# Optimization experiments

Hardware: AMD Instinct MI355X
Metric: run time of the kernel (lower is better)

Reference implementation:

```python
import jax, jax.numpy as jnp
import numpy as np

N, E, B = 20000, 320000, 64
HID, DEPTH, NFREQ = 128, 4, 8
NODE_DIM, EDGE_DIM, SG = 4, 3, 230
TWO_PI = 2.0 * np.pi


def setup_inputs() -> dict:
    key = jax.random.key(0)
    ks = jax.random.split(key, 20)
    inp = {}
    inp["x"] = jax.random.normal(ks[0], (N, NODE_DIM), jnp.float32)
    inp["edge_index"] = jax.random.randint(ks[1], (2, E), 0, N)
    inp["edge_attr"] = jax.random.normal(ks[2], (E, EDGE_DIM), jnp.float32)
    inp["batch"] = jnp.sort(jax.random.randint(ks[3], (N,), 0, B))
    inp["space_group"] = jax.random.randint(ks[4], (B,), 0, SG)
    inp["node_w"] = jax.random.normal(ks[5], (NODE_DIM, HID), jnp.float32) * 0.1
    inp["node_b"] = jnp.zeros((HID,), jnp.float32)
    inp["sg_table"] = jax.random.normal(ks[6], (SG, HID), jnp.float32) * 0.1
    inp["lin_w"] = jax.random.normal(ks[7], (DEPTH, 2 * HID + EDGE_DIM, HID), jnp.float32) * 0.05
    inp["lin_b"] = jnp.zeros((DEPTH, HID), jnp.float32)
    inp["att_w"] = jax.random.normal(ks[8], (DEPTH, 2 * HID + EDGE_DIM), jnp.float32) * 0.05
    inp["att_b"] = jnp.zeros((DEPTH,), jnp.float32)
    inp["fk_w"] = jax.random.normal(ks[9], (DEPTH, NFREQ, HID, HID), jnp.float32) * 0.1
    inp["fk_b"] = jnp.zeros((DEPTH, HID), jnp.float32)
    inp["bn_g"] = jnp.ones((DEPTH, HID), jnp.float32)
    inp["bn_b"] = jnp.zeros((DEPTH, HID), jnp.float32)
    inp["pool_w"] = jax.random.normal(ks[10], (HID,), jnp.float32) * 0.1
    inp["pool_b"] = jnp.zeros((), jnp.float32)
    inp["head_w1"] = jax.random.normal(ks[11], (4, 2 * HID, HID), jnp.float32) * 0.05
    inp["head_b1"] = jnp.zeros((4, HID), jnp.float32)
    for i, (nm, od) in enumerate([("e", 1), ("s", 3), ("c", 7), ("m", 3)]):
        inp[nm + "_w2"] = jax.random.normal(ks[12 + i], (HID, od), jnp.float32) * 0.05
        inp[nm + "_b2"] = jnp.zeros((od,), jnp.float32)
    return inp


def reference(x, edge_index, edge_attr, batch, space_group, node_w, node_b, sg_table,
              lin_w, lin_b, att_w, att_b, fk_w, fk_b, bn_g, bn_b, pool_w, pool_b,
              head_w1, head_b1, e_w2, e_b2, s_w2, s_b2, c_w2, c_b2, m_w2, m_b2):
    src, dst = edge_index[0], edge_index[1]  # x_j = x[src], x_i = x[dst]
    h = x @ node_w + node_b                  # [N, HID]
    sg = sg_table[space_group]               # [B, HID]
    freqs = jnp.arange(1, NFREQ + 1, dtype=h.dtype)
    for l in range(DEPTH):
        # edge conv: gather-concat-linear-sigmoid attention-scatter add
        tmp = jnp.concatenate([h[dst], h[src], edge_attr], axis=-1)   # [E, 2H+3]
        alpha = jax.nn.sigmoid(tmp @ att_w[l] + att_b[l])[:, None]    # [E, 1]
        msg = alpha * (tmp @ lin_w[l] + lin_b[l])                     # [E, H]
        h_conv = jax.ops.segment_sum(msg, dst, num_segments=N)
        # Fourier-Kolmogorov branch
        ang = TWO_PI * freqs[None, :, None] * h[:, None, :]           # [N, K, H]
        h_fk = (jnp.einsum('nki,kio->no', jnp.sin(ang), fk_w[l])
                + jnp.einsum('nki,kio->no', jnp.cos(ang), fk_w[l]) + fk_b[l])
        h = h_conv + h_fk
        # BatchNorm1d (batch statistics, training semantics) + ReLU; dropout = identity (eval)
        mu = h.mean(axis=0)
        var = h.var(axis=0)
        h = (h - mu) / jnp.sqrt(var + 1e-5) * bn_g[l] + bn_b[l]
        h = jax.nn.relu(h)
    # attention pool: softmax over ALL nodes (dim=0), as in the original
    a = jax.nn.softmax(h @ pool_w + pool_b, axis=0)[:, None]          # [N, 1]
    pooled = jax.ops.segment_sum(a * h, batch, num_segments=B)        # [B, H]
    comb = jnp.concatenate([pooled, sg], axis=-1)                     # [B, 2H]

    def head(i, w2, b2):
        z = jax.nn.relu(comb @ head_w1[i] + head_b1[i])
        return z @ w2 + b2

    energy = head(0, e_w2, e_b2)          # [B, 1]
    stability = head(1, s_w2, s_b2)       # [B, 3]
    crystal_system = head(2, c_w2, c_b2)  # [B, 7]
    material_type = head(3, m_w2, m_b2)   # [B, 3]
    return energy, stability, crystal_system, material_type
```

## Files before the change

### kernel.cpp

```cpp
#include <hip/hip_runtime.h>
#include <math.h>

#define HID 128
#define DEPTH 4
#define PSPLIT 16
#define SMAXB 40

typedef _Float16 half8 __attribute__((ext_vector_type(8)));
typedef float f4 __attribute__((ext_vector_type(4)));

__global__ void k_node_embed(const float* __restrict__ x, const float* __restrict__ nw,
                             const float* __restrict__ nb, float* __restrict__ h, int N) {
    int idx = blockIdx.x * blockDim.x + threadIdx.x;
    if (idx >= N * HID) return;
    int n = idx >> 7, c = idx & 127;
    float acc = nb[c];
#pragma unroll
    for (int d = 0; d < 4; ++d) acc += x[n * 4 + d] * nw[d * HID + c];
    h[idx] = acc;
}

__global__ void k_wsplit(const float* __restrict__ fkw, _Float16* __restrict__ whi,
                         _Float16* __restrict__ wlo) {
    __shared__ float sh[64][65];
    int bid = blockIdx.x;
    int l = bid >> 5; int r = bid & 31; int kb = r >> 1; int nbk = r & 1;
    const float* W = fkw + (size_t)l * 131072;
    _Float16* Hl = whi + (size_t)l * 131072;
    _Float16* Ll = wlo + (size_t)l * 131072;
    int k0 = kb * 64, n0 = nbk * 64;
    for (int i = threadIdx.x; i < 4096; i += 256) {
        int kk = i >> 6, nn = i & 63;
        sh[kk][nn] = W[(k0 + kk) * HID + n0 + nn];
    }
    __syncthreads();
    for (int i = threadIdx.x; i < 4096; i += 256) {
        int nn = i >> 6, kk = i & 63;
        float w = sh[kk][nn];
        _Float16 hi = (_Float16)w;
        _Float16 lo = (_Float16)((w - (float)hi) * 2048.f);
        Hl[(n0 + nn) * 1024 + k0 + kk] = hi;
        Ll[(n0 + nn) * 1024 + k0 + kk] = lo;
    }
}

__global__ void k_hist(const int* __restrict__ dst, int* __restrict__ deg, int E) {
    int e = blockIdx.x * 256 + threadIdx.x;
    if (e < E) atomicAdd(&deg[dst[e]], 1);
}

__global__ void k_scan_a(const int* __restrict__ deg, int* __restrict__ bsum, int N) {
    __shared__ int sh[256];
    int i = blockIdx.x * 256 + threadIdx.x;
    sh[threadIdx.x] = (i < N) ? deg[i] : 0;
    __syncthreads();
    for (int off = 128; off > 0; off >>= 1) {
        if (threadIdx.x < (unsigned)off) sh[threadIdx.x] += sh[threadIdx.x + off];
        __syncthreads();
    }
    if (threadIdx.x == 0) bsum[blockIdx.x] = sh[0];
}

__global__ void k_scan_b(int* __restrict__ bsum, int nb) {
    __shared__ int sh[256];
    int v = (threadIdx.x < (unsigned)nb) ? bsum[threadIdx.x] : 0;
    sh[threadIdx.x] = v;
    __syncthreads();
    for (int off = 1; off < 256; off <<= 1) {
        int add = (threadIdx.x >= (unsigned)off) ? sh[threadIdx.x - off] : 0;
        __syncthreads();
        sh[threadIdx.x] += add;
        __syncthreads();
    }
    if (threadIdx.x < (unsigned)nb) bsum[threadIdx.x] = sh[threadIdx.x] - v;
}

__global__ void k_scan_c(const int* __restrict__ deg, const int* __restrict__ bsum,
                         int* __restrict__ offs, int* __restrict__ cursor, int N) {
    __shared__ int sh[256];
    int i = blockIdx.x * 256 + threadIdx.x;
    int v = (i < N) ? deg[i] : 0;
    sh[threadIdx.x] = v;
    __syncthreads();
    for (int off = 1; off < 256; off <<= 1) {
        int add = (threadIdx.x >= (unsigned)off) ? sh[threadIdx.x - off] : 0;
        __syncthreads();
        sh[threadIdx.x] += add;
        __syncthreads();
    }
    int ex = bsum[blockIdx.x] + sh[threadIdx.x] - v;
    if (i < N) { offs[i] = ex; cursor[i] = ex; }
    if (i == N - 1) offs[N] = ex + v;
}

__global__ void k_scatter(const int* __restrict__ src, const int* __restrict__ dst,
                          const float* __restrict__ ea, int* cursor,
                          int* __restrict__ srco, float4* __restrict__ ea3o, int E) {
    int e = blockIdx.x * 256 + threadIdx.x;
    if (e < E) {
        int d = dst[e];
        int p = atomicAdd(&cursor[d], 1);
        srco[p] = src[e];
        float4 q;
        q.x = ea[e * 3 + 0]; q.y = ea[e * 3 + 1]; q.z = ea[e * 3 + 2]; q.w = 0.f;
        ea3o[p] = q;
    }
}

__global__ void k_bstart(const int* __restrict__ batch, int* __restrict__ boffs, int N, int B) {
    int n = blockIdx.x * 256 + threadIdx.x;
    if (n >= N) return;
    int b1 = batch[n];
    if (n == 0) for (int b = 0; b <= b1; ++b) boffs[b] = 0;
    int b2 = (n + 1 < N) ? batch[n + 1] : B;
    for (int b = b1 + 1; b <= b2; ++b) boffs[b] = n + 1;
}

__global__ __launch_bounds__(256) void k_node_lin(const float* __restrict__ h,
                           const float* __restrict__ linw, const float* __restrict__ linb,
                           const float* __restrict__ attw, const float* __restrict__ attb,
                           float* __restrict__ A1, float* __restrict__ A2,
                           float* __restrict__ a1, float* __restrict__ a2, int N) {
    __shared__ float hT[HID][20];
    int nb = blockIdx.x * 16;
    int tid = threadIdx.x;
    for (int i = tid; i < 16 * HID; i += 256) {
        int n = i >> 7, c = i & 127;
        int gn = nb + n;
        hT[c][n] = (gn < N) ? h[gn * HID + c] : 0.f;
    }
    __syncthreads();
    {
        int node = tid >> 4, lane16 = tid & 15;
        float p1 = 0.f, p2 = 0.f;
#pragma unroll
        for (int j = 0; j < 8; ++j) {
            int k = lane16 * 8 + j;
            float hv = hT[k][node];
            p1 += hv * attw[k];
            p2 += hv * attw[128 + k];
        }
        for (int off = 8; off > 0; off >>= 1) {
            p1 += __shfl_down(p1, off, 16);
            p2 += __shfl_down(p2, off, 16);
        }
        int gn = nb + node;
        if (lane16 == 0 && gn < N) {
            a1[gn] = p1 + attb[0];
            a2[gn] = p2;
        }
    }
    int c = tid & 127, r = tid >> 7;
    const float* Wd = linw;
    const float* Ws = linw + 128 * HID;
    float acc1[8] = {0, 0, 0, 0, 0, 0, 0, 0}, acc2[8] = {0, 0, 0, 0, 0, 0, 0, 0};
#pragma unroll 4
    for (int k = 0; k < HID; ++k) {
        float wd = Wd[k * HID + c];
        float ws = Ws[k * HID + c];
        float4 h0 = *(const float4*)&hT[k][r * 8];
        float4 h1 = *(const float4*)&hT[k][r * 8 + 4];
        acc1[0] += h0.x * wd; acc2[0] += h0.x * ws;
        acc1[1] += h0.y * wd; acc2[1] += h0.y * ws;
        acc1[2] += h0.z * wd; acc2[2] += h0.z * ws;
        acc1[3] += h0.w * wd; acc2[3] += h0.w * ws;
        acc1[4] += h1.x * wd; acc2[4] += h1.x * ws;
        acc1[5] += h1.y * wd; acc2[5] += h1.y * ws;
        acc1[6] += h1.z * wd; acc2[6] += h1.z * ws;
        acc1[7] += h1.w * wd; acc2[7] += h1.w * ws;
    }
    float lb = linb[c];
#pragma unroll
    for (int j = 0; j < 8; ++j) {
        int gn = nb + r * 8 + j;
        if (gn < N) {
            A1[(size_t)gn * HID + c] = acc1[j] + lb;
            A2[(size_t)gn * HID + c] = acc2[j];
        }
    }
}

__global__ __launch_bounds__(256) void k_edge(const float* __restrict__ A1,
        const float* __restrict__ A2, const float* __restrict__ a1,
        const float* __restrict__ a2, const int* __restrict__ srco,
        const float4* __restrict__ ea3o, const int* __restrict__ offs,
        const float* __restrict__ linw3, const float* __restrict__ attw3,
        float* __restrict__ hconv, double* __restrict__ stats, int N) {
    __shared__ float part[8][HID + 4];
    int n = blockIdx.x;
    int tid = threadIdx.x;
    if (n == 0) stats[tid] = 0.0;
    int lane32 = tid & 31, slot = tid >> 5;
    int c4 = lane32 * 4;
    float4 w0v = *(const float4*)&linw3[c4];
    float4 w1v = *(const float4*)&linw3[HID + c4];
    float4 w2v = *(const float4*)&linw3[2 * HID + c4];
    float aw0 = attw3[0], aw1 = attw3[1], aw2 = attw3[2];
    float a1n = a1[n];
    float4 A1v = *(const float4*)&A1[(size_t)n * HID + c4];
    float4 acc; acc.x = acc.y = acc.z = acc.w = 0.f;
    int s0 = offs[n], s1 = offs[n + 1];
    for (int idx = s0 + slot; idx < s1; idx += 8) {
        int s = srco[idx];
        float4 q = ea3o[idx];
        float logit = a1n + a2[s] + q.x * aw0 + q.y * aw1 + q.z * aw2;
        float al = 1.f / (1.f + __expf(-logit));
        float4 a2v = *(const float4*)&A2[(size_t)s * HID + c4];
        float4 pre;
        pre.x = A1v.x + a2v.x + q.x * w0v.x + q.y * w1v.x + q.z * w2v.x;
        pre.y = A1v.y + a2v.y + q.x * w0v.y + q.y * w1v.y + q.z * w2v.y;
        pre.z = A1v.z + a2v.z + q.x * w0v.z + q.y * w1v.z + q.z * w2v.z;
        pre.w = A1v.w + a2v.w + q.x * w0v.w + q.y * w1v.w + q.z * w2v.w;
        acc.x += al * pre.x; acc.y += al * pre.y;
        acc.z += al * pre.z; acc.w += al * pre.w;
    }
    *(float4*)&part[slot][c4] = acc;
    __syncthreads();
    if (slot == 0) {
        float4 p = *(const float4*)&part[0][c4];
#pragma unroll
        for (int s = 1; s < 8; ++s) {
            float4 r = *(const float4*)&part[s][c4];
            p.x += r.x; p.y += r.y; p.z += r.z; p.w += r.w;
        }
        *(float4*)&hconv[(size_t)n * HID + c4] = p;
    }
}

#define FK_AST  264
__global__ __launch_bounds__(256) void k_fk(const float* __restrict__ h,
        const _Float16* __restrict__ whi, const _Float16* __restrict__ wlo,
        float* __restrict__ p0, float* __restrict__ p1,
        float* __restrict__ p2, float* __restrict__ p3, int N) {
    __shared__ _Float16 ahi[32 * FK_AST];
    __shared__ _Float16 alo[32 * FK_AST];
    int tid = threadIdx.x;
    int bx = blockIdx.x;
    int nb = (bx >> 2) * 32;
    int ks = bx & 3;
    int kbase = ks * 256;
    int fr0 = kbase >> 7;
    {
        int row = tid >> 3;
        int o8 = tid & 7;
        int gn = nb + row;
        int rc = (gn < N) ? gn : (N - 1);
        const float* hp = h + (size_t)rc * HID + o8 * 8;
        float hv[2][8];
        *(float4*)&hv[0][0] = *(const float4*)hp;
        *(float4*)&hv[0][4] = *(const float4*)(hp + 4);
        *(float4*)&hv[1][0] = *(const float4*)(hp + 64);
        *(float4*)&hv[1][4] = *(const float4*)(hp + 68);
#pragma unroll
        for (int g = 0; g < 2; ++g) {
            float freqf = 6.2831853f * (float)(fr0 + g + 1);
#pragma unroll
            for (int s = 0; s < 2; ++s) {
                half8 vh, vl;
#pragma unroll
                for (int j = 0; j < 8; ++j) {
                    float ang = freqf * hv[s][j] + 0.78539816f;
                    float a = 1.41421356f * __sinf(ang);
                    _Float16 hi = (_Float16)a;
                    vh[j] = hi;
                    vl[j] = (_Float16)((a - (float)hi) * 2048.f);
                }
                int oct = g * 16 + s * 8 + o8;
                *(half8*)&ahi[row * FK_AST + oct * 8] = vh;
                *(half8*)&alo[row * FK_AST + oct * 8] = vl;
            }
        }
    }
    __syncthreads();
    int lane = tid & 63, wv = tid >> 6;
    int quad = lane >> 4, l16 = lane & 15;
    int n0w = wv * 32;
    f4 acc0[2][2], accL[2][2];
#pragma unroll
    for (int mi = 0; mi < 2; ++mi)
#pragma unroll
        for (int ni = 0; ni < 2; ++ni) { acc0[mi][ni] = (f4)(0.f); accL[mi][ni] = (f4)(0.f); }
    const _Float16* bhp0 = whi + (size_t)(n0w + l16) * 1024 + kbase + quad * 8;
    const _Float16* bhp1 = whi + (size_t)(n0w + 16 + l16) * 1024 + kbase + quad * 8;
    const _Float16* blp0 = wlo + (size_t)(n0w + l16) * 1024 + kbase + quad * 8;
    const _Float16* blp1 = wlo + (size_t)(n0w + 16 + l16) * 1024 + kbase + quad * 8;
#pragma unroll 2
    for (int step = 0; step < 8; ++step) {
        int ka = step * 32 + quad * 8;
        half8 ah0 = *(const half8*)&ahi[l16 * FK_AST + ka];
        half8 ah1 = *(const half8*)&ahi[(l16 + 16) * FK_AST + ka];
        half8 al0 = *(const half8*)&alo[l16 * FK_AST + ka];
        half8 al1 = *(const half8*)&alo[(l16 + 16) * FK_AST + ka];
        int ko = step * 32;
        half8 bh0 = *(const half8*)(bhp0 + ko);
        half8 bh1 = *(const half8*)(bhp1 + ko);
        half8 bl0 = *(const half8*)(blp0 + ko);
        half8 bl1 = *(const half8*)(blp1 + ko);
        acc0[0][0] = __builtin_amdgcn_mfma_f32_16x16x32_f16(ah0, bh0, acc0[0][0], 0, 0, 0);
        acc0[0][1] = __builtin_amdgcn_mfma_f32_16x16x32_f16(ah0, bh1, acc0[0][1], 0, 0, 0);
        acc0[1][0] = __builtin_amdgcn_mfma_f32_16x16x32_f16(ah1, bh0, acc0[1][0], 0, 0, 0);
        acc0[1][1] = __builtin_amdgcn_mfma_f32_16x16x32_f16(ah1, bh1, acc0[1][1], 0, 0, 0);
        accL[0][0] = __builtin_amdgcn_mfma_f32_16x16x32_f16(ah0, bl0, accL[0][0], 0, 0, 0);
        accL[0][1] = __builtin_amdgcn_mfma_f32_16x16x32_f16(ah0, bl1, accL[0][1], 0, 0, 0);
        accL[1][0] = __builtin_amdgcn_mfma_f32_16x16x32_f16(ah1, bl0, accL[1][0], 0, 0, 0);
        accL[1][1] = __builtin_amdgcn_mfma_f32_16x16x32_f16(ah1, bl1, accL[1][1], 0, 0, 0);
        accL[0][0] = __builtin_amdgcn_mfma_f32_16x16x32_f16(al0, bh0, accL[0][0], 0, 0, 0);
        accL[0][1] = __builtin_amdgcn_mfma_f32_16x16x32_f16(al0, bh1, accL[0][1], 0, 0, 0);
        accL[1][0] = __builtin_amdgcn_mfma_f32_16x16x32_f16(al1, bh0, accL[1][0], 0, 0, 0);
        accL[1][1] = __builtin_amdgcn_mfma_f32_16x16x32_f16(al1, bh1, accL[1][1], 0, 0, 0);
    }
    float* p = (ks == 0) ? p0 : (ks == 1) ? p1 : (ks == 2) ? p2 : p3;
    const float inv = 1.0f / 2048.0f;
#pragma unroll
    for (int mi = 0; mi < 2; ++mi)
#pragma unroll
        for (int ni = 0; ni < 2; ++ni)
#pragma unroll
            for (int r = 0; r < 4; ++r) {
                int gn = nb + mi * 16 + quad * 4 + r;
                if (gn < N)
                    p[gn * HID + n0w + ni * 16 + l16] = acc0[mi][ni][r] + accL[mi][ni][r] * inv;
            }
}

__global__ __launch_bounds__(256) void k_bn_stats(float* __restrict__ hconv,
                           const float* __restrict__ p0, const float* __restrict__ p1,
                           const float* __restrict__ p2, const float* __restrict__ p3,
                           const float* __restrict__ fkb,
                           double* __restrict__ stats, int N) {
    int tid = threadIdx.x;
    int cq = tid & 31, rg = tid >> 5;
    int c4 = cq * 4;
    float4 bias = *(const float4*)&fkb[c4];
    float s1[4] = {0, 0, 0, 0}, s2[4] = {0, 0, 0, 0};
    for (int n = blockIdx.x * 8 + rg; n < N; n += gridDim.x * 8) {
        size_t idx = (size_t)n * HID + c4;
        float4 a  = *(const float4*)&hconv[idx];
        float4 b0 = *(const float4*)&p0[idx];
        float4 b1 = *(const float4*)&p1[idx];
        float4 b2 = *(const float4*)&p2[idx];
        float4 b3 = *(const float4*)&p3[idx];
        float4 v;
        v.x = a.x + b0.x + b1.x + b2.x + b3.x + bias.x;
        v.y = a.y + b0.y + b1.y + b2.y + b3.y + bias.y;
        v.z = a.z + b0.z + b1.z + b2.z + b3.z + bias.z;
        v.w = a.w + b0.w + b1.w + b2.w + b3.w + bias.w;
        *(float4*)&hconv[idx] = v;
        s1[0] += v.x; s2[0] += v.x * v.x;
        s1[1] += v.y; s2[1] += v.y * v.y;
        s1[2] += v.z; s2[2] += v.z * v.z;
        s1[3] += v.w; s2[3] += v.w * v.w;
    }
#pragma unroll
    for (int j = 0; j < 4; ++j) {
        s1[j] += __shfl_down(s1[j], 32);
        s2[j] += __shfl_down(s2[j], 32);
    }
    __shared__ float sh1[4][32][4], sh2[4][32][4];
    int wv = tid >> 6, lane = tid & 63;
    if (lane < 32) {
#pragma unroll
        for (int j = 0; j < 4; ++j) { sh1[wv][lane][j] = s1[j]; sh2[wv][lane][j] = s2[j]; }
    }
    __syncthreads();
    if (tid < 128) {
        int cq2 = tid >> 2, j2 = tid & 3;
        float t1 = sh1[0][cq2][j2] + sh1[1][cq2][j2] + sh1[2][cq2][j2] + sh1[3][cq2][j2];
        float t2 = sh2[0][cq2][j2] + sh2[1][cq2][j2] + sh2[2][cq2][j2] + sh2[3][cq2][j2];
        int c = cq2 * 4 + j2;
        atomicAdd(&stats[c], (double)t1);
        atomicAdd(&stats[128 + c], (double)t2);
    }
}

__global__ void k_bn_apply(const float* __restrict__ hsum, const double* __restrict__ stats,
                           const float* __restrict__ g, const float* __restrict__ b,
                           const float* __restrict__ pw, const float* __restrict__ pb,
                           float* __restrict__ h, float* __restrict__ s,
                           int do_score, int N) {
    int idx = blockIdx.x * 256 + threadIdx.x;
    int row = idx >> 5, cq = idx & 31;
    int c4 = cq * 4;
    int valid = row < N;
    double invN = 1.0 / (double)N;
    float p = 0.f;
    if (valid) {
        float4 hv = *(const float4*)&hsum[(size_t)row * HID + c4];
        float vin[4] = {hv.x, hv.y, hv.z, hv.w};
        float4 ov;
        float* po = &ov.x;
#pragma unroll
        for (int j = 0; j < 4; ++j) {
            int c = c4 + j;
            float mu = (float)(stats[c] * invN);
            float var = (float)(stats[128 + c] * invN) - mu * mu;
            float inv = 1.f / sqrtf(var + 1e-5f);
            float sc = g[c] * inv;
            float sh = b[c] - mu * sc;
            float oo = fmaxf(vin[j] * sc + sh, 0.f);
            po[j] = oo;
            if (do_score) p += oo * pw[c];
        }
        *(float4*)&h[(size_t)row * HID + c4] = ov;
    }
    if (do_score) {
        for (int off = 16; off > 0; off >>= 1) p += __shfl_down(p, off, 32);
        if ((threadIdx.x & 31) == 0 && valid) s[row] = p + pb[0];
    }
}

__global__ void k_smax1(const float* __restrict__ s, float* __restrict__ mzp, int N) {
    __shared__ float red[256];
    float m = -INFINITY;
    for (int n = blockIdx.x * 256 + threadIdx.x; n < N; n += SMAXB * 256)
        m = fmaxf(m, s[n]);
    red[threadIdx.x] = m;
    __syncthreads();
    for (int off = 128; off > 0; off >>= 1) {
        if (threadIdx.x < (unsigned)off)
            red[threadIdx.x] = fmaxf(red[threadIdx.x], red[threadIdx.x + off]);
        __syncthreads();
    }
    m = red[0];
    __syncthreads();
    float z = 0.f;
    for (int n = blockIdx.x * 256 + threadIdx.x; n < N; n += SMAXB * 256)
        z += __expf(s[n] - m);
    red[threadIdx.x] = z;
    __syncthreads();
    for (int off = 128; off > 0; off >>= 1) {
        if (threadIdx.x < (unsigned)off) red[threadIdx.x] += red[threadIdx.x + off];
        __syncthreads();
    }
    if (threadIdx.x == 0) { mzp[blockIdx.x * 2] = m; mzp[blockIdx.x * 2 + 1] = red[0]; }
}

__device__ __forceinline__ void combine_mz(const float* mzp, float& m, float& Z) {
    m = -INFINITY;
#pragma unroll 8
    for (int i = 0; i < SMAXB; ++i) m = fmaxf(m, mzp[i * 2]);
    Z = 0.f;
#pragma unroll 8
    for (int i = 0; i < SMAXB; ++i) Z += mzp[i * 2 + 1] * __expf(mzp[i * 2] - m);
}

__global__ void k_pool_part(const float* __restrict__ h, const float* __restrict__ s,
                            const float* __restrict__ mzp, const int* __restrict__ boffs,
                            float* __restrict__ part) {
    int b = blockIdx.x >> 4, split = blockIdx.x & (PSPLIT - 1);
    int c = threadIdx.x & 127, half = threadIdx.x >> 7;
    float m, Z;
    combine_mz(mzp, m, Z);
    (void)Z;
    int n0 = boffs[b], n1 = boffs[b + 1];
    float acc = 0.f;
    for (int n = n0 + split * 2 + half; n < n1; n += PSPLIT * 2)
        acc += __expf(s[n] - m) * h[n * HID + c];
    __shared__ float prt[2][HID];
    prt[half][c] = acc;
    __syncthreads();
    if (half == 0) part[(size_t)(b * PSPLIT + split) * HID + c] = prt[0][c] + prt[1][c];
}

__global__ void k_pool_sum(const float* __restrict__ part, const float* __restrict__ mzp,
                           float* __restrict__ pooled) {
    int b = blockIdx.x, c = threadIdx.x;
    float m, Z;
    combine_mz(mzp, m, Z);
    float acc = 0.f;
#pragma unroll
    for (int i = 0; i < PSPLIT; ++i) acc += part[(size_t)(b * PSPLIT + i) * HID + c];
    pooled[b * HID + c] = acc / Z;
}

__global__ __launch_bounds__(256) void k_head(const float* __restrict__ pooled,
                       const float* __restrict__ sg_table,
                       const int* __restrict__ space_group,
                       const float* __restrict__ hw1, const float* __restrict__ hb1,
                       const float* __restrict__ ew2, const float* __restrict__ eb2,
                       const float* __restrict__ sw2, const float* __restrict__ sb2,
                       const float* __restrict__ cw2, const float* __restrict__ cb2,
                       const float* __restrict__ mw2, const float* __restrict__ mb2,
                       float* __restrict__ out, int B) {
    __shared__ float comb[256];
    __shared__ float zred[2][128];
    __shared__ float zsh[128];
    int b = blockIdx.x >> 2, i = blockIdx.x & 3;
    int t = threadIdx.x;
    comb[t] = (t < 128) ? pooled[b * HID + t] : sg_table[space_group[b] * HID + (t - 128)];
    __syncthreads();
    int half = t >> 7, tt = t & 127;
    const float* W = hw1 + ((size_t)i * 256 + half * 128) * HID;
    const float* cb = &comb[half * 128];
    float z = 0.f;
#pragma unroll 8
    for (int k = 0; k < 128; ++k) z += cb[k] * W[k * HID + tt];
    zred[half][tt] = z;
    __syncthreads();
    if (t < 128) zsh[t] = fmaxf(zred[0][t] + zred[1][t] + hb1[i * HID + t], 0.f);
    __syncthreads();
    const int od[4] = {1, 3, 7, 3};
    const int base[4] = {0, 64, 256, 704};
    const float* w2 = (i == 0) ? ew2 : (i == 1) ? sw2 : (i == 2) ? cw2 : mw2;
    const float* b2 = (i == 0) ? eb2 : (i == 1) ? sb2 : (i == 2) ? cb2 : mb2;
    int odi = od[i];
    if (t < odi) {
        float o = b2[t];
        for (int c = 0; c < HID; ++c) o += zsh[c] * w2[c * odi + t];
        out[base[i] + b * odi + t] = o;
    }
}

extern "C" void kernel_launch(void* const* d_in, const int* in_sizes, int n_in,
                              void* d_out, int out_size, void* d_ws, size_t ws_size,
                              hipStream_t stream) {
    const float* x          = (const float*)d_in[0];
    const int*   edge_index = (const int*)d_in[1];
    const float* edge_attr  = (const float*)d_in[2];
    const int*   batch      = (const int*)d_in[3];
    const int*   space_group= (const int*)d_in[4];
    const float* node_w     = (const float*)d_in[5];
    const float* node_b     = (const float*)d_in[6];
    const float* sg_table   = (const float*)d_in[7];
    const float* lin_w      = (const float*)d_in[8];
    const float* lin_b      = (const float*)d_in[9];
    const float* att_w      = (const float*)d_in[10];
    const float* att_b      = (const float*)d_in[11];
    const float* fk_w       = (const float*)d_in[12];
    const float* fk_b       = (const float*)d_in[13];
    const float* bn_g       = (const float*)d_in[14];
    const float* bn_b       = (const float*)d_in[15];
    const float* pool_w     = (const float*)d_in[16];
    const float* pool_b     = (const float*)d_in[17];
    const float* head_w1    = (const float*)d_in[18];
    const float* head_b1    = (const float*)d_in[19];
    const float* ew2 = (const float*)d_in[20]; const float* eb2 = (const float*)d_in[21];
    const float* sw2 = (const float*)d_in[22]; const float* sb2 = (const float*)d_in[23];
    const float* cw2 = (const float*)d_in[24]; const float* cb2 = (const float*)d_in[25];
    const float* mw2 = (const float*)d_in[26]; const float* mb2 = (const float*)d_in[27];
    float* out = (float*)d_out;

    const int N = in_sizes[3];
    const int E = in_sizes[1] / 2;
    const int B = in_sizes[4];
    const int* src = edge_index;
    const int* dst = edge_index + E;

    char* w = (char*)d_ws;
    auto alloc = [&](size_t bytes) { char* p = w; w += (bytes + 255) & ~(size_t)255; return p; };
    float*  h      = (float*)alloc((size_t)N * HID * 4);
    float*  A1     = (float*)alloc((size_t)N * HID * 4);
    float*  A2     = (float*)alloc((size_t)N * HID * 4);
    float*  p2     = (float*)alloc((size_t)N * HID * 4);
    float*  p3     = (float*)alloc((size_t)N * HID * 4);
    float*  hconv  = (float*)alloc((size_t)N * HID * 4);
    float*  a1     = (float*)alloc((size_t)N * 4);
    float*  a2     = (float*)alloc((size_t)N * 4);
    float*  sbuf   = (float*)alloc((size_t)N * 4);
    int*    deg    = (int*)alloc((size_t)N * 4);
    int*    cursor = (int*)alloc((size_t)N * 4);
    int*    offs   = (int*)alloc((size_t)(N + 1) * 4);
    int*    srco   = (int*)alloc((size_t)E * 4);
    float4* ea3o   = (float4*)alloc((size_t)E * 16);
    _Float16* whi  = (_Float16*)alloc((size_t)DEPTH * 1024 * HID * 2);
    _Float16* wlo  = (_Float16*)alloc((size_t)DEPTH * 1024 * HID * 2);
    int*    bsum   = (int*)alloc(256 * 4);
    int*    boffs  = (int*)alloc((size_t)(B + 1) * 4);
    double* stats  = (double*)alloc(256 * 8);
    float*  mzp    = (float*)alloc(SMAXB * 2 * 4);
    float*  part   = (float*)alloc((size_t)B * PSPLIT * HID * 4);
    float*  pooled = (float*)alloc((size_t)B * HID * 4);

    const int nchunk = (N + 255) / 256;
    const int echunk = (E + 255) / 256;

    k_wsplit<<<128, 256, 0, stream>>>(fk_w, whi, wlo);
    hipMemsetAsync(deg, 0, (size_t)N * 4, stream);
    k_hist<<<echunk, 256, 0, stream>>>(dst, deg, E);
    k_scan_a<<<nchunk, 256, 0, stream>>>(deg, bsum, N);
    k_scan_b<<<1, 256, 0, stream>>>(bsum, nchunk);
    k_scan_c<<<nchunk, 256, 0, stream>>>(deg, bsum, offs, cursor, N);
    k_scatter<<<echunk, 256, 0, stream>>>(src, dst, edge_attr, cursor, srco, ea3o, E);
    k_bstart<<<nchunk, 256, 0, stream>>>(batch, boffs, N, B);

    k_node_embed<<<(N * HID + 255) / 256, 256, 0, stream>>>(x, node_w, node_b, h, N);

    for (int l = 0; l < DEPTH; ++l) {
        const float* linw_l = lin_w + (size_t)l * 259 * HID;
        k_node_lin<<<(N + 15) / 16, 256, 0, stream>>>(
            h, linw_l, lin_b + l * HID, att_w + (size_t)l * 259, att_b + l,
            A1, A2, a1, a2, N);
        k_edge<<<N, 256, 0, stream>>>(A1, A2, a1, a2, srco, ea3o, offs,
                                      linw_l + 256 * HID, att_w + (size_t)l * 259 + 256,
                                      hconv, stats, N);
        k_fk<<<((N + 31) / 32) * 4, 256, 0, stream>>>(
            h, whi + (size_t)l * 131072, wlo + (size_t)l * 131072, A1, A2, p2, p3, N);
        k_bn_stats<<<320, 256, 0, stream>>>(hconv, A1, A2, p2, p3, fk_b + l * HID, stats, N);
        k_bn_apply<<<(N * 32 + 255) / 256, 256, 0, stream>>>(
            hconv, stats, bn_g + l * HID, bn_b + l * HID, pool_w, pool_b,
            h, sbuf, (l == DEPTH - 1) ? 1 : 0, N);
    }

    k_smax1<<<SMAXB, 256, 0, stream>>>(sbuf, mzp, N);
    k_pool_part<<<B * PSPLIT, 256, 0, stream>>>(h, sbuf, mzp, boffs, part);
    k_pool_sum<<<B, 128, 0, stream>>>(part, mzp, pooled);
    k_head<<<B * 4, 256, 0, stream>>>(pooled, sg_table, space_group, head_w1, head_b1,
                                      ew2, eb2, sw2, sb2, cw2, cb2, mw2, mb2, out, B);
}
```

Baseline: 712.9 us.

## Retile Fourier-kernel GEMM to 64-row tiles with XOR-swizzled LDS

The k_fk GEMM now processes 64 node rows per block with 512 threads. Each of the 8 waves owns a 16-column strip and reuses one B fragment across four M tiles, where before each wave covered 32x32. The LDS padding is replaced by an XOR swizzle on the 8-half chunk index, which avoids bank conflicts without wasting shared memory. This cuts global weight reads per node but doubles the LDS footprint to 64KB per block, which may limit occupancy.

```diff
diff --git a/kernel.cpp b/kernel.cpp
--- a/kernel.cpp
+++ b/kernel.cpp
@@ -227,16 +227,16 @@
     }
 }
 
-#define FK_AST  264
-__global__ __launch_bounds__(256) void k_fk(const float* __restrict__ h,
+#define FK_MT 64
+__global__ __launch_bounds__(512, 4) void k_fk(const float* __restrict__ h,
         const _Float16* __restrict__ whi, const _Float16* __restrict__ wlo,
         float* __restrict__ p0, float* __restrict__ p1,
         float* __restrict__ p2, float* __restrict__ p3, int N) {
-    __shared__ _Float16 ahi[32 * FK_AST];
-    __shared__ _Float16 alo[32 * FK_AST];
+    __shared__ _Float16 ahi[FK_MT * 256];
+    __shared__ _Float16 alo[FK_MT * 256];
     int tid = threadIdx.x;
     int bx = blockIdx.x;
-    int nb = (bx >> 2) * 32;
+    int nb = (bx >> 2) * FK_MT;
     int ks = bx & 3;
     int kbase = ks * 256;
     int fr0 = kbase >> 7;
@@ -251,6 +251,7 @@
         *(float4*)&hv[0][4] = *(const float4*)(hp + 4);
         *(float4*)&hv[1][0] = *(const float4*)(hp + 64);
         *(float4*)&hv[1][4] = *(const float4*)(hp + 68);
+        int rs = row & 7;
 #pragma unroll
         for (int g = 0; g < 2; ++g) {
             float freqf = 6.2831853f * (float)(fr0 + g + 1);
@@ -265,62 +266,51 @@
                     vh[j] = hi;
                     vl[j] = (_Float16)((a - (float)hi) * 2048.f);
                 }
-                int oct = g * 16 + s * 8 + o8;
-                *(half8*)&ahi[row * FK_AST + oct * 8] = vh;
-                *(half8*)&alo[row * FK_AST + oct * 8] = vl;
+                int oct = (g * 16 + s * 8 + o8) ^ rs;
+                *(half8*)&ahi[row * 256 + oct * 8] = vh;
+                *(half8*)&alo[row * 256 + oct * 8] = vl;
             }
         }
     }
     __syncthreads();
     int lane = tid & 63, wv = tid >> 6;
     int quad = lane >> 4, l16 = lane & 15;
-    int n0w = wv * 32;
-    f4 acc0[2][2], accL[2][2];
-#pragma unroll
-    for (int mi = 0; mi < 2; ++mi)
-#pragma unroll
-        for (int ni = 0; ni < 2; ++ni) { acc0[mi][ni] = (f4)(0.f); accL[mi][ni] = (f4)(0.f); }
-    const _Float16* bhp0 = whi + (size_t)(n0w + l16) * 1024 + kbase + quad * 8;
-    const _Float16* bhp1 = whi + (size_t)(n0w + 16 + l16) * 1024 + kbase + quad * 8;
-    const _Float16* blp0 = wlo + (size_t)(n0w + l16) * 1024 + kbase + quad * 8;
-    const _Float16* blp1 = wlo + (size_t)(n0w + 16 + l16) * 1024 + kbase + quad * 8;
+    int n0w = wv * 16;
+    f4 acc0[4], accL[4];
+#pragma unroll
+    for (int mi = 0; mi < 4; ++mi) { acc0[mi] = (f4)(0.f); accL[mi] = (f4)(0.f); }
+    const _Float16* bhp = whi + (size_t)(n0w + l16) * 1024 + kbase + quad * 8;
+    const _Float16* blp = wlo + (size_t)(n0w + l16) * 1024 + kbase + quad * 8;
+    int rs16 = (l16 & 7) << 3;
 #pragma unroll 2
     for (int step = 0; step < 8; ++step) {
-        int ka = step * 32 + quad * 8;
-        half8 ah0 = *(const half8*)&ahi[l16 * FK_AST + ka];
-        half8 ah1 = *(const half8*)&ahi[(l16 + 16) * FK_AST + ka];
-        half8 al0 = *(const half8*)&alo[l16 * FK_AST + ka];
-        half8 al1 = *(const half8*)&alo[(l16 + 16) * FK_AST + ka];
+        int ka = (step * 32 + quad * 8) ^ rs16;
         int ko = step * 32;
-        half8 bh0 = *(const half8*)(bhp0 + ko);
-        half8 bh1 = *(const half8*)(bhp1 + ko);
-        half8 bl0 = *(const half8*)(blp0 + ko);
-        half8 bl1 = *(const half8*)(blp1 + ko);
-        acc0[0][0] = __builtin_amdgcn_mfma_f32_16x16x32_f16(ah0, bh0, acc0[0][0], 0, 0, 0);
-        acc0[0][1] = __builtin_amdgcn_mfma_f32_16x16x32_f16(ah0, bh1, acc0[0][1], 0, 0, 0);
-        acc0[1][0] = __builtin_amdgcn_mfma_f32_16x16x32_f16(ah1, bh0, acc0[1][0], 0, 0, 0);
-        acc0[1][1] = __builtin_amdgcn_mfma_f32_16x16x32_f16(ah1, bh1, acc0[1][1], 0, 0, 0);
-        accL[0][0] = __builtin_amdgcn_mfma_f32_16x16x32_f16(ah0, bl0, accL[0][0], 0, 0, 0);
-        accL[0][1] = __builtin_amdgcn_mfma_f32_16x16x32_f16(ah0, bl1, accL[0][1], 0, 0, 0);
-        accL[1][0] = __builtin_amdgcn_mfma_f32_16x16x32_f16(ah1, bl0, accL[1][0], 0, 0, 0);
-        accL[1][1] = __builtin_amdgcn_mfma_f32_16x16x32_f16(ah1, bl1, accL[1][1], 0, 0, 0);
-        accL[0][0] = __builtin_amdgcn_mfma_f32_16x16x32_f16(al0, bh0, accL[0][0], 0, 0, 0);
-        accL[0][1] = __builtin_amdgcn_mfma_f32_16x16x32_f16(al0, bh1, accL[0][1], 0, 0, 0);
-        accL[1][0] = __builtin_amdgcn_mfma_f32_16x16x32_f16(al1, bh0, accL[1][0], 0, 0, 0);
-        accL[1][1] = __builtin_amdgcn_mfma_f32_16x16x32_f16(al1, bh1, accL[1][1], 0, 0, 0);
+        half8 bh = *(const half8*)(bhp + ko);
+        half8 bl = *(const half8*)(blp + ko);
+        half8 ah[4], al[4];
+#pragma unroll
+        for (int mi = 0; mi < 4; ++mi) {
+            ah[mi] = *(const half8*)&ahi[(l16 + mi * 16) * 256 + ka];
+            al[mi] = *(const half8*)&alo[(l16 + mi * 16) * 256 + ka];
+        }
+#pragma unroll
+        for (int mi = 0; mi < 4; ++mi) {
+            acc0[mi] = __builtin_amdgcn_mfma_f32_16x16x32_f16(ah[mi], bh, acc0[mi], 0, 0, 0);
+            accL[mi] = __builtin_amdgcn_mfma_f32_16x16x32_f16(ah[mi], bl, accL[mi], 0, 0, 0);
+            accL[mi] = __builtin_amdgcn_mfma_f32_16x16x32_f16(al[mi], bh, accL[mi], 0, 0, 0);
+        }
     }
     float* p = (ks == 0) ? p0 : (ks == 1) ? p1 : (ks == 2) ? p2 : p3;
     const float inv = 1.0f / 2048.0f;
 #pragma unroll
-    for (int mi = 0; mi < 2; ++mi)
-#pragma unroll
-        for (int ni = 0; ni < 2; ++ni)
-#pragma unroll
-            for (int r = 0; r < 4; ++r) {
-                int gn = nb + mi * 16 + quad * 4 + r;
-                if (gn < N)
-                    p[gn * HID + n0w + ni * 16 + l16] = acc0[mi][ni][r] + accL[mi][ni][r] * inv;
-            }
+    for (int mi = 0; mi < 4; ++mi)
+#pragma unroll
+        for (int r = 0; r < 4; ++r) {
+            int gn = nb + mi * 16 + quad * 4 + r;
+            if (gn < N)
+                p[gn * HID + n0w + l16] = acc0[mi][r] + accL[mi][r] * inv;
+        }
 }
 
 __global__ __launch_bounds__(256) void k_bn_stats(float* __restrict__ hconv,
@@ -593,7 +583,7 @@
         k_edge<<<N, 256, 0, stream>>>(A1, A2, a1, a2, srco, ea3o, offs,
                                       linw_l + 256 * HID, att_w + (size_t)l * 259 + 256,
                                       hconv, stats, N);
-        k_fk<<<((N + 31) / 32) * 4, 256, 0, stream>>>(
+        k_fk<<<((N + 63) / 64) * 4, 512, 0, stream>>>(
             h, whi + (size_t)l * 131072, wlo + (size_t)l * 131072, A1, A2, p2, p3, N);
         k_bn_stats<<<320, 256, 0, stream>>>(hconv, A1, A2, p2, p3, fk_b + l * HID, stats, N);
         k_bn_apply<<<(N * 32 + 255) / 256, 256, 0, stream>>>(
```

Measured after the change: 668.4 us. -6.2%, faster.
